# Kernel optimization log

Hardware: AMD Instinct MI355X
Metric: run time of the kernel (lower is better)

The kernel has to match this reference:

```python
import jax, jax.numpy as jnp
import numpy as np

B, D, H, W, K = 512, 128, 30, 30, 5
TEMP = 1.0


def _ln(x, g, b, eps=1e-5):
    m = x.mean(-1, keepdims=True)
    v = ((x - m) ** 2).mean(-1, keepdims=True)
    return (x - m) / jnp.sqrt(v + eps) * g + b


def setup_inputs() -> dict:
    key = jax.random.key(0)
    ks = jax.random.split(key, 8)
    f32 = jnp.float32
    def n(k, shape, s=0.05):
        return jax.random.normal(k, shape, f32) * s
    return {
        "features": jax.random.normal(ks[0], (B, D, H, W), f32),
        "clue_queries": jax.random.normal(ks[1], (K, D), f32),
        "wq": n(ks[2], (D, D)), "bq": jnp.zeros((D,), f32),
        "wk": n(ks[3], (D, D)), "bk": jnp.zeros((D,), f32),
        "wv": n(ks[4], (D, D)), "bv": jnp.zeros((D,), f32),
        "sw1": n(ks[5], (D // 2, D + 1)), "sb1": jnp.zeros((D // 2,), f32),
        "sw2": n(ks[6], (1, D // 2), 0.1), "sb2": jnp.full((1,), -1.0, f32),
        "qn_g": jnp.ones((D,), f32), "qn_b": jnp.zeros((D,), f32),
        "fn_g": jnp.ones((D,), f32), "fn_b": jnp.zeros((D,), f32),
    }


def reference(features, clue_queries, wq, bq, wk, bk, wv, bv,
              sw1, sb1, sw2, sb2, qn_g, qn_b, fn_g, fn_b):
    Bv, Dv, Hv, Wv = features.shape
    HW = Hv * Wv
    # (B, HW, D) normalized features
    feat = _ln(features.transpose(0, 2, 3, 1).reshape(Bv, HW, Dv), fn_g, fn_b)
    # Queries / keys / values: key & value projections are loop-invariant in the
    # original (recomputed identically each iteration) so we hoist them.
    q = _ln(clue_queries, qn_g, qn_b) @ wq.T + bq          # (K, D)
    kp = feat @ wk.T + bk                                   # (B, HW, D)
    v = feat @ wv.T + bv                                    # (B, HW, D)
    scale = jnp.sqrt(jnp.asarray(Dv, feat.dtype))
    base = jnp.einsum('kd,bnd->bkn', q, kp) / scale         # (B, K, HW)

    rows = (jnp.arange(HW) // Wv).astype(feat.dtype)
    cols = (jnp.arange(HW) % Wv).astype(feat.dtype)
    max_ent = jnp.log(jnp.asarray(HW + 1e-6, feat.dtype))
    gkey = jax.random.key(42)

    cum = jnp.ones((Bv, HW), feat.dtype)
    cents, attns, stops = [], [], []
    for k in range(K):
        s = base[:, k] + jnp.log(jnp.clip(cum, 1e-6, None))
        s = jnp.clip(s, -50.0, 50.0)
        u = jnp.clip(jax.random.uniform(jax.random.fold_in(gkey, k), s.shape,
                                        feat.dtype), 1e-10, 1.0 - 1e-10)
        g = -jnp.log(-jnp.log(u))
        noisy = jnp.clip((s + g) / max(TEMP, 1e-10), -50.0, 50.0)
        attn = jax.nn.softmax(noisy, axis=-1)               # (B, HW)
        # soft centroid (row, col)
        cents.append(jnp.stack([(attn * rows).sum(-1), (attn * cols).sum(-1)], -1))
        attended = jnp.einsum('bn,bnd->bd', attn, v)        # (B, D)
        ac = jnp.clip(attn, 1e-10, None)
        ent = -(ac * jnp.log(ac)).sum(-1, keepdims=True) / max_ent
        h = jax.nn.gelu(jnp.concatenate([attended, ent], -1) @ sw1.T + sb1,
                        approximate=False)
        stops.append((h @ sw2.T + sb2)[..., 0])
        attns.append(attn)
        cum = jnp.clip(cum * (1.0 - 0.9 * jax.lax.stop_gradient(attn)), 1e-6, None)

    centroids = jnp.stack(cents, 1)                         # (B, K, 2)
    attention_maps = jnp.stack(attns, 1).reshape(Bv, K, Hv, Wv)
    stop_logits = jnp.stack(stops, 1)                       # (B, K)
    return centroids, attention_maps, stop_logits
```

## Files before the change

kernel.cpp:

```cpp
#include <hip/hip_runtime.h>
#include <stdint.h>
#include <math.h>

namespace {
constexpr int Bn = 512, Dn = 128, Wn = 30, Kn = 5;
constexpr int HWn = 900;
constexpr int TQ  = 225;

constexpr size_t OFF_A  = 0;
constexpr size_t OFF_SA = OFF_A + (size_t)Kn * Dn;
constexpr size_t OFF_C0 = OFF_SA + 8;

constexpr size_t OUT_CENT = 0;
constexpr size_t OUT_ATTN = (size_t)Bn * Kn * 2;
constexpr size_t OUT_STOP = OUT_ATTN + (size_t)Bn * Kn * HWn;
}

struct FoldedKeys { uint32_t k1[5]; uint32_t k2[5]; };

__host__ __device__ static inline uint32_t rotl32(uint32_t x, int d) {
  return (x << d) | (x >> (32 - d));
}

__host__ __device__ static inline void threefry2x32(uint32_t k1, uint32_t k2,
                                                    uint32_t& x0, uint32_t& x1) {
  uint32_t k3 = k1 ^ k2 ^ 0x1BD11BDAu;
  x0 += k1; x1 += k2;
#define TF_R(rot) { x0 += x1; x1 = rotl32(x1, rot); x1 ^= x0; }
  TF_R(13) TF_R(15) TF_R(26) TF_R(6)   x0 += k2; x1 += k3 + 1u;
  TF_R(17) TF_R(29) TF_R(16) TF_R(24)  x0 += k3; x1 += k1 + 2u;
  TF_R(13) TF_R(15) TF_R(26) TF_R(6)   x0 += k1; x1 += k2 + 3u;
  TF_R(17) TF_R(29) TF_R(16) TF_R(24)  x0 += k2; x1 += k3 + 4u;
  TF_R(13) TF_R(15) TF_R(26) TF_R(6)   x0 += k3; x1 += k1 + 5u;
#undef TF_R
}

__device__ static inline float wsum(float v) {
#pragma unroll
  for (int o = 32; o; o >>= 1) v += __shfl_xor(v, o, 64);
  return v;
}
__device__ static inline float wmaxr(float v) {
#pragma unroll
  for (int o = 32; o; o >>= 1) v = fmaxf(v, __shfl_xor(v, o, 64));
  return v;
}
__device__ static inline float bsum4(float v, float* scr) {
  v = wsum(v);
  if ((threadIdx.x & 63) == 0) scr[threadIdx.x >> 6] = v;
  __syncthreads();
  float r = scr[0] + scr[1] + scr[2] + scr[3];
  __syncthreads();
  return r;
}
__device__ static inline float bmax4(float v, float* scr) {
  v = wmaxr(v);
  if ((threadIdx.x & 63) == 0) scr[threadIdx.x >> 6] = v;
  __syncthreads();
  float r = fmaxf(fmaxf(scr[0], scr[1]), fmaxf(scr[2], scr[3]));
  __syncthreads();
  return r;
}
__device__ static inline float bsum2(float v, float* scr) {
  v = wsum(v);
  if ((threadIdx.x & 63) == 0) scr[threadIdx.x >> 6] = v;
  __syncthreads();
  float r = scr[0] + scr[1];
  __syncthreads();
  return r;
}

__global__ __launch_bounds__(128) void k_prep(
    const float* __restrict__ clue, const float* __restrict__ wq,
    const float* __restrict__ bq, const float* __restrict__ wk,
    const float* __restrict__ bk, const float* __restrict__ qn_g,
    const float* __restrict__ qn_b, const float* __restrict__ fn_g,
    const float* __restrict__ fn_b, float* __restrict__ ws) {
  __shared__ float scr[2];
  __shared__ float lnc[Dn], qrow[Dn], qkrow[Dn];
  const int k = blockIdx.x, t = threadIdx.x;
  float xv = clue[(size_t)k * Dn + t];
  float m = bsum2(xv, scr) * (1.0f / Dn);
  float dd = xv - m;
  float var = bsum2(dd * dd, scr) * (1.0f / Dn);
  float r = 1.0f / sqrtf(var + 1e-5f);
  lnc[t] = dd * r * qn_g[t] + qn_b[t];
  __syncthreads();
  {
    float acc = bq[t];
    const float* wr = wq + (size_t)t * Dn;
    for (int e = 0; e < Dn; ++e) acc += lnc[e] * wr[e];
    qrow[t] = acc;
  }
  __syncthreads();
  {
    float acc = 0.f;
    for (int d = 0; d < Dn; ++d) acc += qrow[d] * wk[(size_t)d * Dn + t];
    qkrow[t] = acc;
    ws[OFF_A + (size_t)k * Dn + t] = fn_g[t] * acc;
  }
  __syncthreads();
  float sa = bsum2(fn_g[t] * qkrow[t], scr);
  float c0 = bsum2(fn_b[t] * qkrow[t] + qrow[t] * bk[t], scr);
  if (t == 0) {
    ws[OFF_SA + k] = sa;
    ws[OFF_C0 + k] = c0;
  }
}

__global__ __launch_bounds__(256) void k_all(
    const float* __restrict__ x, const float* __restrict__ ws,
    const float* __restrict__ wv, const float* __restrict__ bv,
    const float* __restrict__ sw1, const float* __restrict__ sb1,
    const float* __restrict__ sw2, const float* __restrict__ sb2,
    const float* __restrict__ fn_g, const float* __restrict__ fn_b,
    float* __restrict__ out, FoldedKeys keys) {
  __shared__ float Al[Kn * Dn];
  __shared__ float wl[Kn * HWn];
  __shared__ float dots[Kn * Dn];
  __shared__ float att[Kn * Dn];
  __shared__ float hbuf[Kn * 64];
  __shared__ float scr4[4];
  __shared__ float scr16[16];
  __shared__ float caL[8], entL[8];
  const int b = blockIdx.x, t = threadIdx.x;
  for (int i = t; i < Kn * Dn; i += 256) Al[i] = ws[OFF_A + i];
  __syncthreads();
  const bool act = (t < TQ);
  const float4* xq = (const float4*)(x + (size_t)b * Dn * HWn);

  float sm[4] = {0, 0, 0, 0}, sq[4] = {0, 0, 0, 0};
  float sd[5][4] = {};
  {
    const float4* xt = xq + (act ? t : 0);
    for (int e0 = 0; e0 < Dn; e0 += 8) {
      float4 vb[8];
#pragma unroll
      for (int j = 0; j < 8; ++j) vb[j] = xt[(size_t)(e0 + j) * TQ];
#pragma unroll
      for (int j = 0; j < 8; ++j) {
        const int e = e0 + j;
        float a0 = Al[e], a1 = Al[Dn + e], a2 = Al[2 * Dn + e],
              a3 = Al[3 * Dn + e], a4 = Al[4 * Dn + e];
        float vv[4] = {vb[j].x, vb[j].y, vb[j].z, vb[j].w};
#pragma unroll
        for (int c = 0; c < 4; ++c) {
          sm[c] += vv[c];
          sq[c] += vv[c] * vv[c];
          sd[0][c] += vv[c] * a0; sd[1][c] += vv[c] * a1;
          sd[2][c] += vv[c] * a2; sd[3][c] += vv[c] * a3;
          sd[4][c] += vv[c] * a4;
        }
      }
    }
  }
  float SA[5], C0[5];
#pragma unroll
  for (int k = 0; k < 5; ++k) { SA[k] = ws[OFF_SA + k]; C0[k] = ws[OFF_C0 + k]; }
  float r[4], mr[4], base[5][4], cum[4], rw[4], cl[4];
#pragma unroll
  for (int c = 0; c < 4; ++c) {
    float m = sm[c] * (1.0f / Dn);
    float var = sq[c] * (1.0f / Dn) - m * m;
    r[c] = 1.0f / sqrtf(var + 1e-5f);
    mr[c] = m * r[c];
    cum[c] = 1.0f;
    int n = 4 * t + c;
    rw[c] = (float)(n / Wn);
    cl[c] = (float)(n % Wn);
#pragma unroll
    for (int k = 0; k < 5; ++k)
      base[k][c] = (r[c] * (sd[k][c] - m * SA[k]) + C0[k]) * 0.08838834764831844f;
  }

  for (int k = 0; k < 5; ++k) {
    const uint32_t fk1 = keys.k1[k], fk2 = keys.k2[k];
    float noisy[4];
#pragma unroll
    for (int c = 0; c < 4; ++c) {
      if (act) {
        float s = base[k][c] + logf(cum[c]);
        s = fminf(fmaxf(s, -50.f), 50.f);
        uint32_t j = (uint32_t)(b * HWn + 4 * t + c);
        uint32_t x0 = 0u, x1 = j;
        threefry2x32(fk1, fk2, x0, x1);
        uint32_t bits = x0 ^ x1;
        float u = __uint_as_float((bits >> 9) | 0x3f800000u) - 1.0f;
        u = fmaxf(u, 1e-10f);
        float g = -logf(-logf(u));
        noisy[c] = fminf(fmaxf(s + g, -50.f), 50.f);
      } else {
        noisy[c] = -1e30f;
      }
    }
    float lm = fmaxf(fmaxf(noisy[0], noisy[1]), fmaxf(noisy[2], noisy[3]));
    const float M = bmax4(lm, scr4);
    float p[4], ls = 0.f;
#pragma unroll
    for (int c = 0; c < 4; ++c) {
      p[c] = act ? expf(noisy[c] - M) : 0.f;
      ls += p[c];
    }
    const float Z = bsum4(ls, scr4);
    const float inv = 1.0f / Z;
    float red[4] = {0, 0, 0, 0};
    float av[4];
#pragma unroll
    for (int c = 0; c < 4; ++c) {
      float a = p[c] * inv;
      av[c] = a;
      if (act) {
        red[0] += a * rw[c];
        red[1] += a * cl[c];
        float ac = fmaxf(a, 1e-10f);
        red[2] += ac * logf(ac);
        red[3] += a * mr[c];
        cum[c] = fmaxf(cum[c] * (1.0f - 0.9f * a), 1e-6f);
      }
    }
    if (act) {
      *(float4*)&out[OUT_ATTN + ((size_t)(b * Kn + k)) * HWn + 4 * t] =
          make_float4(av[0], av[1], av[2], av[3]);
      *(float4*)&wl[(size_t)k * HWn + 4 * t] =
          make_float4(av[0] * r[0], av[1] * r[1], av[2] * r[2], av[3] * r[3]);
    }
#pragma unroll
    for (int j2 = 0; j2 < 4; ++j2) red[j2] = wsum(red[j2]);
    if ((t & 63) == 0) {
      int w = t >> 6;
      scr16[w * 4 + 0] = red[0]; scr16[w * 4 + 1] = red[1];
      scr16[w * 4 + 2] = red[2]; scr16[w * 4 + 3] = red[3];
    }
    __syncthreads();
    if (t == 0) {
      float cr = scr16[0] + scr16[4] + scr16[8] + scr16[12];
      float cc = scr16[1] + scr16[5] + scr16[9] + scr16[13];
      float ea = scr16[2] + scr16[6] + scr16[10] + scr16[14];
      float ca = scr16[3] + scr16[7] + scr16[11] + scr16[15];
      out[OUT_CENT + ((size_t)(b * Kn + k)) * 2 + 0] = cr;
      out[OUT_CENT + ((size_t)(b * Kn + k)) * 2 + 1] = cc;
      caL[k] = ca;
      entL[k] = -ea / 6.802394763324311f;
    }
    __syncthreads();
  }

  const int lane = t & 63, wid = t >> 6;
  for (int gi = 0; gi < 4; ++gi) {
    const int g = 15 - (gi * 4 + wid);
    const int d0 = g * 8;
    float acc[8][5] = {};
    for (int i0 = 0; i0 < 4; ++i0) {
      const int i = i0 * 64 + lane;
      if (i < TQ) {
        float4 v[8];
#pragma unroll
        for (int j = 0; j < 8; ++j) v[j] = xq[(size_t)(d0 + j) * TQ + i];
        float w4[5][4];
#pragma unroll
        for (int k = 0; k < 5; ++k) {
          float4 wv4 = *(const float4*)&wl[k * HWn + 4 * i];
          w4[k][0] = wv4.x; w4[k][1] = wv4.y; w4[k][2] = wv4.z; w4[k][3] = wv4.w;
        }
#pragma unroll
        for (int j = 0; j < 8; ++j)
#pragma unroll
          for (int k = 0; k < 5; ++k)
            acc[j][k] += v[j].x * w4[k][0] + v[j].y * w4[k][1] +
                         v[j].z * w4[k][2] + v[j].w * w4[k][3];
      }
    }
#pragma unroll
    for (int j = 0; j < 8; ++j)
#pragma unroll
      for (int k = 0; k < 5; ++k) {
        float s = wsum(acc[j][k]);
        if (lane == 0) dots[k * Dn + d0 + j] = s;
      }
  }
  __syncthreads();

  float* af = Al;
  for (int i = t; i < Kn * Dn; i += 256) {
    int k = i >> 7, e = i & 127;
    af[i] = fn_g[e] * (dots[i] - caL[k]) + fn_b[e];
  }
  __syncthreads();
  for (int i = t; i < Kn * Dn; i += 256) {
    int k = i >> 7, d2 = i & 127;
    const float4* wr = (const float4*)(wv + (size_t)d2 * Dn);
    const float4* afq = (const float4*)&af[k << 7];
    float s = bv[d2];
    for (int e = 0; e < Dn / 4; ++e) {
      float4 a = afq[e], w = wr[e];
      s += a.x * w.x + a.y * w.y + a.z * w.z + a.w * w.w;
    }
    att[i] = s;
  }
  __syncthreads();
  for (int i = t; i < Kn * 64; i += 256) {
    int k = i >> 6, j = i & 63;
    const float* sr = sw1 + (size_t)j * (Dn + 1);
    float s = sb1[j];
    for (int e = 0; e < Dn; ++e) s += sr[e] * att[(k << 7) + e];
    s += entL[k] * sr[Dn];
    hbuf[i] = s * (erff(s * 0.7071067811865475f) + 1.0f) * 0.5f;
  }
  __syncthreads();
  if (t < Kn) {
    float s = sb2[0];
    for (int j = 0; j < 64; ++j) s += hbuf[(t << 6) + j] * sw2[j];
    out[OUT_STOP + (size_t)b * Kn + t] = s;
  }
}

extern "C" void kernel_launch(void* const* d_in, const int* in_sizes, int n_in,
                              void* d_out, int out_size, void* d_ws, size_t ws_size,
                              hipStream_t stream) {
  (void)in_sizes; (void)n_in; (void)out_size; (void)ws_size;
  const float* features = (const float*)d_in[0];
  const float* clue     = (const float*)d_in[1];
  const float* wq       = (const float*)d_in[2];
  const float* bq       = (const float*)d_in[3];
  const float* wk       = (const float*)d_in[4];
  const float* bk       = (const float*)d_in[5];
  const float* wv       = (const float*)d_in[6];
  const float* bv       = (const float*)d_in[7];
  const float* sw1      = (const float*)d_in[8];
  const float* sb1      = (const float*)d_in[9];
  const float* sw2      = (const float*)d_in[10];
  const float* sb2      = (const float*)d_in[11];
  const float* qn_g     = (const float*)d_in[12];
  const float* qn_b     = (const float*)d_in[13];
  const float* fn_g     = (const float*)d_in[14];
  const float* fn_b     = (const float*)d_in[15];
  float* ws  = (float*)d_ws;
  float* out = (float*)d_out;

  FoldedKeys fk;
  for (int k = 0; k < Kn; ++k) {
    uint32_t x0 = 0u, x1 = (uint32_t)k;
    threefry2x32(0u, 42u, x0, x1);
    fk.k1[k] = x0; fk.k2[k] = x1;
  }

  hipLaunchKernelGGL(k_prep, dim3(Kn), dim3(128), 0, stream,
                     clue, wq, bq, wk, bk, qn_g, qn_b, fn_g, fn_b, ws);
  hipLaunchKernelGGL(k_all, dim3(Bn), dim3(256), 0, stream,
                     features, ws, wv, bv, sw1, sb1, sw2, sb2, fn_g, fn_b,
                     out, fk);
}
```

Baseline: 124.9 us.

## Split fused kernel into base-score pass and attention/projection pass

Splits the single per-batch kernel into two launches. The first uses 1024 blocks (two per batch), each thread handling two pixels, to compute layernorm statistics and base scores; it writes r, m*r to the workspace and the base scores into the attention output buffer. The second kernel reads those back, runs the Gumbel-softmax loop and the value projection, and visits batches in reverse order with the d-group order flipped, probably to hit feature data still in cache from the first pass. This buys more parallelism for the bandwidth-heavy feature scan at the cost of an extra launch, extra global round trips, and a second full read of the features.

After: 265.2 us. 2.12x slower.

```diff
diff --git a/kernel.cpp b/kernel.cpp
--- a/kernel.cpp
+++ b/kernel.cpp
@@ -10,6 +10,8 @@
 constexpr size_t OFF_A  = 0;
 constexpr size_t OFF_SA = OFF_A + (size_t)Kn * Dn;
 constexpr size_t OFF_C0 = OFF_SA + 8;
+constexpr size_t OFF_R  = OFF_C0 + 8;
+constexpr size_t OFF_MR = OFF_R + (size_t)Bn * HWn;
 
 constexpr size_t OUT_CENT = 0;
 constexpr size_t OUT_ATTN = (size_t)Bn * Kn * 2;
@@ -108,80 +110,114 @@
   }
 }
 
-__global__ __launch_bounds__(256) void k_all(
+__global__ __launch_bounds__(256) void k_base(const float* __restrict__ x,
+                                              float* __restrict__ ws,
+                                              float* __restrict__ out) {
+  __shared__ float Al[Kn * Dn];
+  const int b = blockIdx.y, half = blockIdx.x, t = threadIdx.x;
+  for (int i = t; i < Kn * Dn; i += 256) Al[i] = ws[OFF_A + i];
+  __syncthreads();
+  const bool act = (t < TQ);
+  const int P = half * TQ + (act ? t : 0);
+  const float2* xt = (const float2*)(x + (size_t)b * Dn * HWn) + P;
+
+  float sm[2] = {0, 0}, sq[2] = {0, 0};
+  float sd[5][2] = {};
+  for (int e0 = 0; e0 < Dn; e0 += 8) {
+    float2 vb[8];
+#pragma unroll
+    for (int j = 0; j < 8; ++j) vb[j] = xt[(size_t)(e0 + j) * (HWn / 2)];
+#pragma unroll
+    for (int j = 0; j < 8; ++j) {
+      const int e = e0 + j;
+      float a0 = Al[e], a1 = Al[Dn + e], a2 = Al[2 * Dn + e],
+            a3 = Al[3 * Dn + e], a4 = Al[4 * Dn + e];
+      float vv[2] = {vb[j].x, vb[j].y};
+#pragma unroll
+      for (int c = 0; c < 2; ++c) {
+        sm[c] += vv[c];
+        sq[c] += vv[c] * vv[c];
+        sd[0][c] += vv[c] * a0; sd[1][c] += vv[c] * a1;
+        sd[2][c] += vv[c] * a2; sd[3][c] += vv[c] * a3;
+        sd[4][c] += vv[c] * a4;
+      }
+    }
+  }
+  if (!act) return;
+  float SA[5], C0[5];
+#pragma unroll
+  for (int k = 0; k < 5; ++k) { SA[k] = ws[OFF_SA + k]; C0[k] = ws[OFF_C0 + k]; }
+  float r[2], m[2];
+#pragma unroll
+  for (int c = 0; c < 2; ++c) {
+    m[c] = sm[c] * (1.0f / Dn);
+    float var = sq[c] * (1.0f / Dn) - m[c] * m[c];
+    r[c] = 1.0f / sqrtf(var + 1e-5f);
+  }
+  const int n0 = 2 * P;
+  *(float2*)&ws[OFF_R + (size_t)b * HWn + n0] = make_float2(r[0], r[1]);
+  *(float2*)&ws[OFF_MR + (size_t)b * HWn + n0] =
+      make_float2(m[0] * r[0], m[1] * r[1]);
+#pragma unroll
+  for (int k = 0; k < 5; ++k) {
+    float b0 = (r[0] * (sd[k][0] - m[0] * SA[k]) + C0[k]) * 0.08838834764831844f;
+    float b1 = (r[1] * (sd[k][1] - m[1] * SA[k]) + C0[k]) * 0.08838834764831844f;
+    *(float2*)&out[OUT_ATTN + ((size_t)(b * Kn + k)) * HWn + n0] =
+        make_float2(b0, b1);
+  }
+}
+
+__global__ __launch_bounds__(256) void k_rest(
     const float* __restrict__ x, const float* __restrict__ ws,
     const float* __restrict__ wv, const float* __restrict__ bv,
     const float* __restrict__ sw1, const float* __restrict__ sb1,
     const float* __restrict__ sw2, const float* __restrict__ sb2,
     const float* __restrict__ fn_g, const float* __restrict__ fn_b,
     float* __restrict__ out, FoldedKeys keys) {
-  __shared__ float Al[Kn * Dn];
   __shared__ float wl[Kn * HWn];
   __shared__ float dots[Kn * Dn];
+  __shared__ float af[Kn * Dn];
   __shared__ float att[Kn * Dn];
   __shared__ float hbuf[Kn * 64];
   __shared__ float scr4[4];
   __shared__ float scr16[16];
   __shared__ float caL[8], entL[8];
-  const int b = blockIdx.x, t = threadIdx.x;
-  for (int i = t; i < Kn * Dn; i += 256) Al[i] = ws[OFF_A + i];
-  __syncthreads();
+  const int b = Bn - 1 - blockIdx.x;
+  const int t = threadIdx.x;
   const bool act = (t < TQ);
-  const float4* xq = (const float4*)(x + (size_t)b * Dn * HWn);
-
-  float sm[4] = {0, 0, 0, 0}, sq[4] = {0, 0, 0, 0};
-  float sd[5][4] = {};
+  const int t4 = 4 * (act ? t : 0);
+
+  float r[4], mr[4], cum[4], rw[4], cl[4];
   {
-    const float4* xt = xq + (act ? t : 0);
-    for (int e0 = 0; e0 < Dn; e0 += 8) {
-      float4 vb[8];
-#pragma unroll
-      for (int j = 0; j < 8; ++j) vb[j] = xt[(size_t)(e0 + j) * TQ];
-#pragma unroll
-      for (int j = 0; j < 8; ++j) {
-        const int e = e0 + j;
-        float a0 = Al[e], a1 = Al[Dn + e], a2 = Al[2 * Dn + e],
-              a3 = Al[3 * Dn + e], a4 = Al[4 * Dn + e];
-        float vv[4] = {vb[j].x, vb[j].y, vb[j].z, vb[j].w};
-#pragma unroll
-        for (int c = 0; c < 4; ++c) {
-          sm[c] += vv[c];
-          sq[c] += vv[c] * vv[c];
-          sd[0][c] += vv[c] * a0; sd[1][c] += vv[c] * a1;
-          sd[2][c] += vv[c] * a2; sd[3][c] += vv[c] * a3;
-          sd[4][c] += vv[c] * a4;
-        }
-      }
-    }
-  }
-  float SA[5], C0[5];
-#pragma unroll
-  for (int k = 0; k < 5; ++k) { SA[k] = ws[OFF_SA + k]; C0[k] = ws[OFF_C0 + k]; }
-  float r[4], mr[4], base[5][4], cum[4], rw[4], cl[4];
-#pragma unroll
-  for (int c = 0; c < 4; ++c) {
-    float m = sm[c] * (1.0f / Dn);
-    float var = sq[c] * (1.0f / Dn) - m * m;
-    r[c] = 1.0f / sqrtf(var + 1e-5f);
-    mr[c] = m * r[c];
-    cum[c] = 1.0f;
-    int n = 4 * t + c;
-    rw[c] = (float)(n / Wn);
-    cl[c] = (float)(n % Wn);
-#pragma unroll
-    for (int k = 0; k < 5; ++k)
-      base[k][c] = (r[c] * (sd[k][c] - m * SA[k]) + C0[k]) * 0.08838834764831844f;
-  }
-
+    float4 rv = make_float4(0, 0, 0, 0), mv = make_float4(0, 0, 0, 0);
+    if (act) {
+      rv = *(const float4*)&ws[OFF_R + (size_t)b * HWn + t4];
+      mv = *(const float4*)&ws[OFF_MR + (size_t)b * HWn + t4];
+    }
+    r[0] = rv.x; r[1] = rv.y; r[2] = rv.z; r[3] = rv.w;
+    mr[0] = mv.x; mr[1] = mv.y; mr[2] = mv.z; mr[3] = mv.w;
+#pragma unroll
+    for (int c = 0; c < 4; ++c) {
+      cum[c] = 1.0f;
+      int n = t4 + c;
+      rw[c] = (float)(n / Wn);
+      cl[c] = (float)(n % Wn);
+    }
+  }
   for (int k = 0; k < 5; ++k) {
     const uint32_t fk1 = keys.k1[k], fk2 = keys.k2[k];
+    float base4[4] = {0, 0, 0, 0};
+    if (act) {
+      float4 bv4 = *(const float4*)&out[OUT_ATTN + ((size_t)(b * Kn + k)) * HWn + t4];
+      base4[0] = bv4.x; base4[1] = bv4.y; base4[2] = bv4.z; base4[3] = bv4.w;
+    }
     float noisy[4];
 #pragma unroll
     for (int c = 0; c < 4; ++c) {
       if (act) {
-        float s = base[k][c] + logf(cum[c]);
+        float s = base4[c] + logf(cum[c]);
         s = fminf(fmaxf(s, -50.f), 50.f);
-        uint32_t j = (uint32_t)(b * HWn + 4 * t + c);
+        uint32_t j = (uint32_t)(b * HWn + t4 + c);
         uint32_t x0 = 0u, x1 = j;
         threefry2x32(fk1, fk2, x0, x1);
         uint32_t bits = x0 ^ x1;
@@ -219,9 +255,9 @@
       }
     }
     if (act) {
-      *(float4*)&out[OUT_ATTN + ((size_t)(b * Kn + k)) * HWn + 4 * t] =
+      *(float4*)&out[OUT_ATTN + ((size_t)(b * Kn + k)) * HWn + t4] =
           make_float4(av[0], av[1], av[2], av[3]);
-      *(float4*)&wl[(size_t)k * HWn + 4 * t] =
+      *(float4*)&wl[(size_t)k * HWn + t4] =
           make_float4(av[0] * r[0], av[1] * r[1], av[2] * r[2], av[3] * r[3]);
     }
 #pragma unroll
@@ -246,8 +282,9 @@
   }
 
   const int lane = t & 63, wid = t >> 6;
+  const float4* xq = (const float4*)(x + (size_t)b * Dn * HWn);
   for (int gi = 0; gi < 4; ++gi) {
-    const int g = 15 - (gi * 4 + wid);
+    const int g = gi * 4 + wid;
     const int d0 = g * 8;
     float acc[8][5] = {};
     for (int i0 = 0; i0 < 4; ++i0) {
@@ -280,7 +317,6 @@
   }
   __syncthreads();
 
-  float* af = Al;
   for (int i = t; i < Kn * Dn; i += 256) {
     int k = i >> 7, e = i & 127;
     af[i] = fn_g[e] * (dots[i] - caL[k]) + fn_b[e];
@@ -346,7 +382,9 @@
 
   hipLaunchKernelGGL(k_prep, dim3(Kn), dim3(128), 0, stream,
                      clue, wq, bq, wk, bk, qn_g, qn_b, fn_g, fn_b, ws);
-  hipLaunchKernelGGL(k_all, dim3(Bn), dim3(256), 0, stream,
+  hipLaunchKernelGGL(k_base, dim3(2, Bn), dim3(256), 0, stream,
+                     features, ws, out);
+  hipLaunchKernelGGL(k_rest, dim3(Bn), dim3(256), 0, stream,
                      features, ws, wv, bv, sw1, sb1, sw2, sb2, fn_g, fn_b,
                      out, fk);
 }
```

## Use 1024-thread blocks with one pixel per thread and fixed-shift softmax

Applied to the files above, without the earlier changes.

Grows the per-batch block from 256 threads (four pixels each, float4 loads) to 1024 threads with one pixel per thread and scalar loads. The separate block max reduction is dropped: since noisy is clamped to at most 50, exp(noisy-50) is used directly. All softmax statistics (Z, centroids, entropy through a log-sum identity, mean term) are fused into one five-way reduction, which removes two barrier pairs per step and the per-pixel log. This trades wider vector loads and per-thread ILP for more parallelism and fewer barriers, with a risk of underflow when all logits are far below 50.

Result: slower. 163.8 us (+31.1%).

```diff
diff --git a/kernel.cpp b/kernel.cpp
--- a/kernel.cpp
+++ b/kernel.cpp
@@ -5,7 +5,6 @@
 namespace {
 constexpr int Bn = 512, Dn = 128, Wn = 30, Kn = 5;
 constexpr int HWn = 900;
-constexpr int TQ  = 225;
 
 constexpr size_t OFF_A  = 0;
 constexpr size_t OFF_SA = OFF_A + (size_t)Kn * Dn;
@@ -39,27 +38,6 @@
 #pragma unroll
   for (int o = 32; o; o >>= 1) v += __shfl_xor(v, o, 64);
   return v;
-}
-__device__ static inline float wmaxr(float v) {
-#pragma unroll
-  for (int o = 32; o; o >>= 1) v = fmaxf(v, __shfl_xor(v, o, 64));
-  return v;
-}
-__device__ static inline float bsum4(float v, float* scr) {
-  v = wsum(v);
-  if ((threadIdx.x & 63) == 0) scr[threadIdx.x >> 6] = v;
-  __syncthreads();
-  float r = scr[0] + scr[1] + scr[2] + scr[3];
-  __syncthreads();
-  return r;
-}
-__device__ static inline float bmax4(float v, float* scr) {
-  v = wmaxr(v);
-  if ((threadIdx.x & 63) == 0) scr[threadIdx.x >> 6] = v;
-  __syncthreads();
-  float r = fmaxf(fmaxf(scr[0], scr[1]), fmaxf(scr[2], scr[3]));
-  __syncthreads();
-  return r;
 }
 __device__ static inline float bsum2(float v, float* scr) {
   v = wsum(v);
@@ -108,7 +86,7 @@
   }
 }
 
-__global__ __launch_bounds__(256) void k_all(
+__global__ __launch_bounds__(1024) void k_all(
     const float* __restrict__ x, const float* __restrict__ ws,
     const float* __restrict__ wv, const float* __restrict__ bv,
     const float* __restrict__ sw1, const float* __restrict__ sb1,
@@ -120,158 +98,127 @@
   __shared__ float dots[Kn * Dn];
   __shared__ float att[Kn * Dn];
   __shared__ float hbuf[Kn * 64];
-  __shared__ float scr4[4];
-  __shared__ float scr16[16];
+  __shared__ float scrS[16 * 5];
+  __shared__ float bcZ[4];
   __shared__ float caL[8], entL[8];
   const int b = blockIdx.x, t = threadIdx.x;
-  for (int i = t; i < Kn * Dn; i += 256) Al[i] = ws[OFF_A + i];
-  __syncthreads();
-  const bool act = (t < TQ);
-  const float4* xq = (const float4*)(x + (size_t)b * Dn * HWn);
-
-  float sm[4] = {0, 0, 0, 0}, sq[4] = {0, 0, 0, 0};
-  float sd[5][4] = {};
-  {
-    const float4* xt = xq + (act ? t : 0);
-    for (int e0 = 0; e0 < Dn; e0 += 8) {
-      float4 vb[8];
-#pragma unroll
-      for (int j = 0; j < 8; ++j) vb[j] = xt[(size_t)(e0 + j) * TQ];
-#pragma unroll
-      for (int j = 0; j < 8; ++j) {
+  if (t < Kn * Dn) Al[t] = ws[OFF_A + t];
+  __syncthreads();
+  const bool act = (t < HWn);
+  const float* xb = x + (size_t)b * Dn * HWn;
+
+  float sm = 0.f, sq = 0.f;
+  float sd[5] = {};
+  {
+    const float* xt = xb + (act ? t : 0);
+    for (int e0 = 0; e0 < Dn; e0 += 4) {
+      float vb[4];
+#pragma unroll
+      for (int j = 0; j < 4; ++j) vb[j] = xt[(size_t)(e0 + j) * HWn];
+#pragma unroll
+      for (int j = 0; j < 4; ++j) {
         const int e = e0 + j;
-        float a0 = Al[e], a1 = Al[Dn + e], a2 = Al[2 * Dn + e],
-              a3 = Al[3 * Dn + e], a4 = Al[4 * Dn + e];
-        float vv[4] = {vb[j].x, vb[j].y, vb[j].z, vb[j].w};
-#pragma unroll
-        for (int c = 0; c < 4; ++c) {
-          sm[c] += vv[c];
-          sq[c] += vv[c] * vv[c];
-          sd[0][c] += vv[c] * a0; sd[1][c] += vv[c] * a1;
-          sd[2][c] += vv[c] * a2; sd[3][c] += vv[c] * a3;
-          sd[4][c] += vv[c] * a4;
-        }
-      }
-    }
-  }
-  float SA[5], C0[5];
-#pragma unroll
-  for (int k = 0; k < 5; ++k) { SA[k] = ws[OFF_SA + k]; C0[k] = ws[OFF_C0 + k]; }
-  float r[4], mr[4], base[5][4], cum[4], rw[4], cl[4];
-#pragma unroll
-  for (int c = 0; c < 4; ++c) {
-    float m = sm[c] * (1.0f / Dn);
-    float var = sq[c] * (1.0f / Dn) - m * m;
-    r[c] = 1.0f / sqrtf(var + 1e-5f);
-    mr[c] = m * r[c];
-    cum[c] = 1.0f;
-    int n = 4 * t + c;
-    rw[c] = (float)(n / Wn);
-    cl[c] = (float)(n % Wn);
+        float v = vb[j];
+        sm += v;
+        sq += v * v;
+        sd[0] += v * Al[e];
+        sd[1] += v * Al[Dn + e];
+        sd[2] += v * Al[2 * Dn + e];
+        sd[3] += v * Al[3 * Dn + e];
+        sd[4] += v * Al[4 * Dn + e];
+      }
+    }
+  }
+  float base[5], r, mr;
+  {
+    float m = sm * (1.0f / Dn);
+    float var = sq * (1.0f / Dn) - m * m;
+    r = 1.0f / sqrtf(var + 1e-5f);
+    mr = m * r;
 #pragma unroll
     for (int k = 0; k < 5; ++k)
-      base[k][c] = (r[c] * (sd[k][c] - m * SA[k]) + C0[k]) * 0.08838834764831844f;
-  }
+      base[k] = (r * (sd[k] - m * ws[OFF_SA + k]) + ws[OFF_C0 + k]) *
+                0.08838834764831844f;
+  }
+  const float rw = (float)(t / Wn), cl = (float)(t % Wn);
+  float cum = 1.0f;
 
   for (int k = 0; k < 5; ++k) {
     const uint32_t fk1 = keys.k1[k], fk2 = keys.k2[k];
-    float noisy[4];
-#pragma unroll
-    for (int c = 0; c < 4; ++c) {
-      if (act) {
-        float s = base[k][c] + logf(cum[c]);
-        s = fminf(fmaxf(s, -50.f), 50.f);
-        uint32_t j = (uint32_t)(b * HWn + 4 * t + c);
-        uint32_t x0 = 0u, x1 = j;
-        threefry2x32(fk1, fk2, x0, x1);
-        uint32_t bits = x0 ^ x1;
-        float u = __uint_as_float((bits >> 9) | 0x3f800000u) - 1.0f;
-        u = fmaxf(u, 1e-10f);
-        float g = -logf(-logf(u));
-        noisy[c] = fminf(fmaxf(s + g, -50.f), 50.f);
-      } else {
-        noisy[c] = -1e30f;
-      }
-    }
-    float lm = fmaxf(fmaxf(noisy[0], noisy[1]), fmaxf(noisy[2], noisy[3]));
-    const float M = bmax4(lm, scr4);
-    float p[4], ls = 0.f;
-#pragma unroll
-    for (int c = 0; c < 4; ++c) {
-      p[c] = act ? expf(noisy[c] - M) : 0.f;
-      ls += p[c];
-    }
-    const float Z = bsum4(ls, scr4);
-    const float inv = 1.0f / Z;
-    float red[4] = {0, 0, 0, 0};
-    float av[4];
-#pragma unroll
-    for (int c = 0; c < 4; ++c) {
-      float a = p[c] * inv;
-      av[c] = a;
-      if (act) {
-        red[0] += a * rw[c];
-        red[1] += a * cl[c];
-        float ac = fmaxf(a, 1e-10f);
-        red[2] += ac * logf(ac);
-        red[3] += a * mr[c];
-        cum[c] = fmaxf(cum[c] * (1.0f - 0.9f * a), 1e-6f);
-      }
-    }
+    float noisy;
     if (act) {
-      *(float4*)&out[OUT_ATTN + ((size_t)(b * Kn + k)) * HWn + 4 * t] =
-          make_float4(av[0], av[1], av[2], av[3]);
-      *(float4*)&wl[(size_t)k * HWn + 4 * t] =
-          make_float4(av[0] * r[0], av[1] * r[1], av[2] * r[2], av[3] * r[3]);
-    }
-#pragma unroll
-    for (int j2 = 0; j2 < 4; ++j2) red[j2] = wsum(red[j2]);
+      float s = base[k] + logf(cum);
+      s = fminf(fmaxf(s, -50.f), 50.f);
+      uint32_t x0 = 0u, x1 = (uint32_t)(b * HWn + t);
+      threefry2x32(fk1, fk2, x0, x1);
+      uint32_t bits = x0 ^ x1;
+      float u = __uint_as_float((bits >> 9) | 0x3f800000u) - 1.0f;
+      u = fmaxf(u, 1e-10f);
+      float g = -logf(-logf(u));
+      noisy = fminf(fmaxf(s + g, -50.f), 50.f);
+    } else {
+      noisy = -1e30f;
+    }
+    const float pl = noisy - 50.0f;
+    const float p = expf(pl);
+    float P[5];
+    P[0] = p; P[1] = p * rw; P[2] = p * cl; P[3] = p * pl; P[4] = p * mr;
+#pragma unroll
+    for (int q = 0; q < 5; ++q) P[q] = wsum(P[q]);
     if ((t & 63) == 0) {
       int w = t >> 6;
-      scr16[w * 4 + 0] = red[0]; scr16[w * 4 + 1] = red[1];
-      scr16[w * 4 + 2] = red[2]; scr16[w * 4 + 3] = red[3];
+#pragma unroll
+      for (int q = 0; q < 5; ++q) scrS[w * 5 + q] = P[q];
     }
     __syncthreads();
     if (t == 0) {
-      float cr = scr16[0] + scr16[4] + scr16[8] + scr16[12];
-      float cc = scr16[1] + scr16[5] + scr16[9] + scr16[13];
-      float ea = scr16[2] + scr16[6] + scr16[10] + scr16[14];
-      float ca = scr16[3] + scr16[7] + scr16[11] + scr16[15];
-      out[OUT_CENT + ((size_t)(b * Kn + k)) * 2 + 0] = cr;
-      out[OUT_CENT + ((size_t)(b * Kn + k)) * 2 + 1] = cc;
-      caL[k] = ca;
-      entL[k] = -ea / 6.802394763324311f;
+      float S0 = 0, S1 = 0, S2 = 0, S3 = 0, S4 = 0;
+#pragma unroll
+      for (int w = 0; w < 16; ++w) {
+        S0 += scrS[w * 5 + 0]; S1 += scrS[w * 5 + 1]; S2 += scrS[w * 5 + 2];
+        S3 += scrS[w * 5 + 3]; S4 += scrS[w * 5 + 4];
+      }
+      const float invZ = 1.0f / S0;
+      out[OUT_CENT + ((size_t)(b * Kn + k)) * 2 + 0] = S1 * invZ;
+      out[OUT_CENT + ((size_t)(b * Kn + k)) * 2 + 1] = S2 * invZ;
+      caL[k] = S4 * invZ;
+      entL[k] = -(S3 * invZ - logf(S0)) * 0.14700905142472002f;
+      bcZ[0] = invZ;
     }
     __syncthreads();
+    const float invZ = bcZ[0];
+    if (act) {
+      float a = p * invZ;
+      out[OUT_ATTN + ((size_t)(b * Kn + k)) * HWn + t] = a;
+      wl[(size_t)k * HWn + t] = a * r;
+      cum = fmaxf(cum * (1.0f - 0.9f * a), 1e-6f);
+    }
+    __syncthreads();
   }
 
   const int lane = t & 63, wid = t >> 6;
-  for (int gi = 0; gi < 4; ++gi) {
-    const int g = 15 - (gi * 4 + wid);
-    const int d0 = g * 8;
-    float acc[8][5] = {};
-    for (int i0 = 0; i0 < 4; ++i0) {
+#pragma unroll
+  for (int h = 0; h < 2; ++h) {
+    const int d0 = wid * 8 + h * 4;
+    float acc[4][5] = {};
+    for (int i0 = 0; i0 < 15; ++i0) {
       const int i = i0 * 64 + lane;
-      if (i < TQ) {
-        float4 v[8];
-#pragma unroll
-        for (int j = 0; j < 8; ++j) v[j] = xq[(size_t)(d0 + j) * TQ + i];
-        float w4[5][4];
-#pragma unroll
-        for (int k = 0; k < 5; ++k) {
-          float4 wv4 = *(const float4*)&wl[k * HWn + 4 * i];
-          w4[k][0] = wv4.x; w4[k][1] = wv4.y; w4[k][2] = wv4.z; w4[k][3] = wv4.w;
+      if (i < HWn) {
+        float v[4];
+#pragma unroll
+        for (int j = 0; j < 4; ++j) v[j] = xb[(size_t)(d0 + j) * HWn + i];
+        float w0 = wl[i], w1 = wl[HWn + i], w2 = wl[2 * HWn + i],
+              w3 = wl[3 * HWn + i], w4 = wl[4 * HWn + i];
+#pragma unroll
+        for (int j = 0; j < 4; ++j) {
+          acc[j][0] += v[j] * w0; acc[j][1] += v[j] * w1;
+          acc[j][2] += v[j] * w2; acc[j][3] += v[j] * w3;
+          acc[j][4] += v[j] * w4;
         }
-#pragma unroll
-        for (int j = 0; j < 8; ++j)
-#pragma unroll
-          for (int k = 0; k < 5; ++k)
-            acc[j][k] += v[j].x * w4[k][0] + v[j].y * w4[k][1] +
-                         v[j].z * w4[k][2] + v[j].w * w4[k][3];
-      }
-    }
-#pragma unroll
-    for (int j = 0; j < 8; ++j)
+      }
+    }
+#pragma unroll
+    for (int j = 0; j < 4; ++j)
 #pragma unroll
       for (int k = 0; k < 5; ++k) {
         float s = wsum(acc[j][k]);
@@ -281,13 +228,13 @@
   __syncthreads();
 
   float* af = Al;
-  for (int i = t; i < Kn * Dn; i += 256) {
-    int k = i >> 7, e = i & 127;
-    af[i] = fn_g[e] * (dots[i] - caL[k]) + fn_b[e];
-  }
-  __syncthreads();
-  for (int i = t; i < Kn * Dn; i += 256) {
-    int k = i >> 7, d2 = i & 127;
+  if (t < Kn * Dn) {
+    int k = t >> 7, e = t & 127;
+    af[t] = fn_g[e] * (dots[t] - caL[k]) + fn_b[e];
+  }
+  __syncthreads();
+  if (t < Kn * Dn) {
+    int k = t >> 7, d2 = t & 127;
     const float4* wr = (const float4*)(wv + (size_t)d2 * Dn);
     const float4* afq = (const float4*)&af[k << 7];
     float s = bv[d2];
@@ -295,16 +242,16 @@
       float4 a = afq[e], w = wr[e];
       s += a.x * w.x + a.y * w.y + a.z * w.z + a.w * w.w;
     }
-    att[i] = s;
-  }
-  __syncthreads();
-  for (int i = t; i < Kn * 64; i += 256) {
-    int k = i >> 6, j = i & 63;
+    att[t] = s;
+  }
+  __syncthreads();
+  if (t < Kn * 64) {
+    int k = t >> 6, j = t & 63;
     const float* sr = sw1 + (size_t)j * (Dn + 1);
     float s = sb1[j];
     for (int e = 0; e < Dn; ++e) s += sr[e] * att[(k << 7) + e];
     s += entL[k] * sr[Dn];
-    hbuf[i] = s * (erff(s * 0.7071067811865475f) + 1.0f) * 0.5f;
+    hbuf[t] = s * (erff(s * 0.7071067811865475f) + 1.0f) * 0.5f;
   }
   __syncthreads();
   if (t < Kn) {
@@ -346,7 +293,7 @@
 
   hipLaunchKernelGGL(k_prep, dim3(Kn), dim3(128), 0, stream,
                      clue, wq, bq, wk, bk, qn_g, qn_b, fn_g, fn_b, ws);
-  hipLaunchKernelGGL(k_all, dim3(Bn), dim3(256), 0, stream,
+  hipLaunchKernelGGL(k_all, dim3(Bn), dim3(1024), 0, stream,
                      features, ws, wv, bv, sw1, sb1, sw2, sb2, fn_g, fn_b,
                      out, fk);
 }
```

## Fuse softmax max/sum/centroid/entropy reductions into single pass with fixed shift

Applied to the files above, without the earlier changes.

Replaces the data-dependent max reduction with a fixed shift of 50, since noisy logits are clipped to [-50,50]. Sum, centroid, entropy and mean terms all come from one fused block reduction over unnormalised exponentials, with entropy rebuilt algebraically as E[pl] - log Z. This removes two block-wide barrier reductions per clue step. The feature-stats loop also switches to a register double-buffered prefetch of 4 rows instead of batches of 8. Risks: exp of values near -100 can underflow for very negative logits, and dropping the 1e-10 clamp in the entropy term changes numerics slightly.

Result: slower. 183.7 us (+47.1%).

```diff
diff --git a/kernel.cpp b/kernel.cpp
--- a/kernel.cpp
+++ b/kernel.cpp
@@ -39,27 +39,6 @@
 #pragma unroll
   for (int o = 32; o; o >>= 1) v += __shfl_xor(v, o, 64);
   return v;
-}
-__device__ static inline float wmaxr(float v) {
-#pragma unroll
-  for (int o = 32; o; o >>= 1) v = fmaxf(v, __shfl_xor(v, o, 64));
-  return v;
-}
-__device__ static inline float bsum4(float v, float* scr) {
-  v = wsum(v);
-  if ((threadIdx.x & 63) == 0) scr[threadIdx.x >> 6] = v;
-  __syncthreads();
-  float r = scr[0] + scr[1] + scr[2] + scr[3];
-  __syncthreads();
-  return r;
-}
-__device__ static inline float bmax4(float v, float* scr) {
-  v = wmaxr(v);
-  if ((threadIdx.x & 63) == 0) scr[threadIdx.x >> 6] = v;
-  __syncthreads();
-  float r = fmaxf(fmaxf(scr[0], scr[1]), fmaxf(scr[2], scr[3]));
-  __syncthreads();
-  return r;
 }
 __device__ static inline float bsum2(float v, float* scr) {
   v = wsum(v);
@@ -120,8 +99,8 @@
   __shared__ float dots[Kn * Dn];
   __shared__ float att[Kn * Dn];
   __shared__ float hbuf[Kn * 64];
-  __shared__ float scr4[4];
-  __shared__ float scr16[16];
+  __shared__ float scrS[4 * 5];
+  __shared__ float bc[4];
   __shared__ float caL[8], entL[8];
   const int b = blockIdx.x, t = threadIdx.x;
   for (int i = t; i < Kn * Dn; i += 256) Al[i] = ws[OFF_A + i];
@@ -133,16 +112,20 @@
   float sd[5][4] = {};
   {
     const float4* xt = xq + (act ? t : 0);
-    for (int e0 = 0; e0 < Dn; e0 += 8) {
-      float4 vb[8];
-#pragma unroll
-      for (int j = 0; j < 8; ++j) vb[j] = xt[(size_t)(e0 + j) * TQ];
-#pragma unroll
-      for (int j = 0; j < 8; ++j) {
+    float4 cur[4], nxt[4];
+#pragma unroll
+    for (int j = 0; j < 4; ++j) cur[j] = xt[(size_t)j * TQ];
+    for (int e0 = 0; e0 < Dn; e0 += 4) {
+      if (e0 + 4 < Dn) {
+#pragma unroll
+        for (int j = 0; j < 4; ++j) nxt[j] = xt[(size_t)(e0 + 4 + j) * TQ];
+      }
+#pragma unroll
+      for (int j = 0; j < 4; ++j) {
         const int e = e0 + j;
         float a0 = Al[e], a1 = Al[Dn + e], a2 = Al[2 * Dn + e],
               a3 = Al[3 * Dn + e], a4 = Al[4 * Dn + e];
-        float vv[4] = {vb[j].x, vb[j].y, vb[j].z, vb[j].w};
+        float vv[4] = {cur[j].x, cur[j].y, cur[j].z, cur[j].w};
 #pragma unroll
         for (int c = 0; c < 4; ++c) {
           sm[c] += vv[c];
@@ -152,95 +135,92 @@
           sd[4][c] += vv[c] * a4;
         }
       }
-    }
-  }
-  float SA[5], C0[5];
-#pragma unroll
-  for (int k = 0; k < 5; ++k) { SA[k] = ws[OFF_SA + k]; C0[k] = ws[OFF_C0 + k]; }
+#pragma unroll
+      for (int j = 0; j < 4; ++j) cur[j] = nxt[j];
+    }
+  }
   float r[4], mr[4], base[5][4], cum[4], rw[4], cl[4];
-#pragma unroll
-  for (int c = 0; c < 4; ++c) {
-    float m = sm[c] * (1.0f / Dn);
-    float var = sq[c] * (1.0f / Dn) - m * m;
-    r[c] = 1.0f / sqrtf(var + 1e-5f);
-    mr[c] = m * r[c];
-    cum[c] = 1.0f;
-    int n = 4 * t + c;
-    rw[c] = (float)(n / Wn);
-    cl[c] = (float)(n % Wn);
-#pragma unroll
-    for (int k = 0; k < 5; ++k)
-      base[k][c] = (r[c] * (sd[k][c] - m * SA[k]) + C0[k]) * 0.08838834764831844f;
+  {
+    float SA[5], C0[5];
+#pragma unroll
+    for (int k = 0; k < 5; ++k) { SA[k] = ws[OFF_SA + k]; C0[k] = ws[OFF_C0 + k]; }
+#pragma unroll
+    for (int c = 0; c < 4; ++c) {
+      float m = sm[c] * (1.0f / Dn);
+      float var = sq[c] * (1.0f / Dn) - m * m;
+      r[c] = 1.0f / sqrtf(var + 1e-5f);
+      mr[c] = m * r[c];
+      cum[c] = 1.0f;
+      int n = 4 * t + c;
+      rw[c] = (float)(n / Wn);
+      cl[c] = (float)(n % Wn);
+#pragma unroll
+      for (int k = 0; k < 5; ++k)
+        base[k][c] = (r[c] * (sd[k][c] - m * SA[k]) + C0[k]) *
+                     0.08838834764831844f;
+    }
   }
 
   for (int k = 0; k < 5; ++k) {
     const uint32_t fk1 = keys.k1[k], fk2 = keys.k2[k];
-    float noisy[4];
+    float pv[4], P[5] = {0, 0, 0, 0, 0};
 #pragma unroll
     for (int c = 0; c < 4; ++c) {
+      float noisy;
       if (act) {
         float s = base[k][c] + logf(cum[c]);
         s = fminf(fmaxf(s, -50.f), 50.f);
-        uint32_t j = (uint32_t)(b * HWn + 4 * t + c);
-        uint32_t x0 = 0u, x1 = j;
+        uint32_t x0 = 0u, x1 = (uint32_t)(b * HWn + 4 * t + c);
         threefry2x32(fk1, fk2, x0, x1);
         uint32_t bits = x0 ^ x1;
         float u = __uint_as_float((bits >> 9) | 0x3f800000u) - 1.0f;
         u = fmaxf(u, 1e-10f);
         float g = -logf(-logf(u));
-        noisy[c] = fminf(fmaxf(s + g, -50.f), 50.f);
+        noisy = fminf(fmaxf(s + g, -50.f), 50.f);
       } else {
-        noisy[c] = -1e30f;
-      }
-    }
-    float lm = fmaxf(fmaxf(noisy[0], noisy[1]), fmaxf(noisy[2], noisy[3]));
-    const float M = bmax4(lm, scr4);
-    float p[4], ls = 0.f;
-#pragma unroll
-    for (int c = 0; c < 4; ++c) {
-      p[c] = act ? expf(noisy[c] - M) : 0.f;
-      ls += p[c];
-    }
-    const float Z = bsum4(ls, scr4);
-    const float inv = 1.0f / Z;
-    float red[4] = {0, 0, 0, 0};
-    float av[4];
-#pragma unroll
-    for (int c = 0; c < 4; ++c) {
-      float a = p[c] * inv;
-      av[c] = a;
-      if (act) {
-        red[0] += a * rw[c];
-        red[1] += a * cl[c];
-        float ac = fmaxf(a, 1e-10f);
-        red[2] += ac * logf(ac);
-        red[3] += a * mr[c];
-        cum[c] = fmaxf(cum[c] * (1.0f - 0.9f * a), 1e-6f);
-      }
-    }
-    if (act) {
-      *(float4*)&out[OUT_ATTN + ((size_t)(b * Kn + k)) * HWn + 4 * t] =
-          make_float4(av[0], av[1], av[2], av[3]);
-      *(float4*)&wl[(size_t)k * HWn + 4 * t] =
-          make_float4(av[0] * r[0], av[1] * r[1], av[2] * r[2], av[3] * r[3]);
-    }
-#pragma unroll
-    for (int j2 = 0; j2 < 4; ++j2) red[j2] = wsum(red[j2]);
+        noisy = -1e30f;
+      }
+      float pl = noisy - 50.0f;
+      float p = expf(pl);
+      pv[c] = p;
+      P[0] += p; P[1] += p * rw[c]; P[2] += p * cl[c];
+      P[3] += p * pl; P[4] += p * mr[c];
+    }
+#pragma unroll
+    for (int q = 0; q < 5; ++q) P[q] = wsum(P[q]);
     if ((t & 63) == 0) {
       int w = t >> 6;
-      scr16[w * 4 + 0] = red[0]; scr16[w * 4 + 1] = red[1];
-      scr16[w * 4 + 2] = red[2]; scr16[w * 4 + 3] = red[3];
+#pragma unroll
+      for (int q = 0; q < 5; ++q) scrS[w * 5 + q] = P[q];
     }
     __syncthreads();
     if (t == 0) {
-      float cr = scr16[0] + scr16[4] + scr16[8] + scr16[12];
-      float cc = scr16[1] + scr16[5] + scr16[9] + scr16[13];
-      float ea = scr16[2] + scr16[6] + scr16[10] + scr16[14];
-      float ca = scr16[3] + scr16[7] + scr16[11] + scr16[15];
-      out[OUT_CENT + ((size_t)(b * Kn + k)) * 2 + 0] = cr;
-      out[OUT_CENT + ((size_t)(b * Kn + k)) * 2 + 1] = cc;
-      caL[k] = ca;
-      entL[k] = -ea / 6.802394763324311f;
+      float S0 = 0, S1 = 0, S2 = 0, S3 = 0, S4 = 0;
+#pragma unroll
+      for (int w = 0; w < 4; ++w) {
+        S0 += scrS[w * 5 + 0]; S1 += scrS[w * 5 + 1]; S2 += scrS[w * 5 + 2];
+        S3 += scrS[w * 5 + 3]; S4 += scrS[w * 5 + 4];
+      }
+      const float invZ = 1.0f / S0;
+      out[OUT_CENT + ((size_t)(b * Kn + k)) * 2 + 0] = S1 * invZ;
+      out[OUT_CENT + ((size_t)(b * Kn + k)) * 2 + 1] = S2 * invZ;
+      caL[k] = S4 * invZ;
+      entL[k] = -(S3 * invZ - logf(S0)) * 0.14700905142472002f;
+      bc[0] = invZ;
+    }
+    __syncthreads();
+    const float invZ = bc[0];
+    if (act) {
+      float a0 = pv[0] * invZ, a1 = pv[1] * invZ,
+            a2 = pv[2] * invZ, a3 = pv[3] * invZ;
+      *(float4*)&out[OUT_ATTN + ((size_t)(b * Kn + k)) * HWn + 4 * t] =
+          make_float4(a0, a1, a2, a3);
+      *(float4*)&wl[(size_t)k * HWn + 4 * t] =
+          make_float4(a0 * r[0], a1 * r[1], a2 * r[2], a3 * r[3]);
+      cum[0] = fmaxf(cum[0] * (1.0f - 0.9f * a0), 1e-6f);
+      cum[1] = fmaxf(cum[1] * (1.0f - 0.9f * a1), 1e-6f);
+      cum[2] = fmaxf(cum[2] * (1.0f - 0.9f * a2), 1e-6f);
+      cum[3] = fmaxf(cum[3] * (1.0f - 0.9f * a3), 1e-6f);
     }
     __syncthreads();
   }
```
